# Kernel tuning notes

Measured on AMD Instinct MI355X. Metric: run time of the kernel, lower is better.

The kernel has to match this reference:

```python
import jax, jax.numpy as jnp
import numpy as np

D_MODEL = 1024
N_HEADS = 16
D_K = D_MODEL // N_HEADS
SCALE = float(np.sqrt(D_K))


def setup_inputs() -> dict:
    key = jax.random.key(0)
    ks = jax.random.split(key, 11)
    B, L, D = 2, 2048, D_MODEL
    s = 1.0 / np.sqrt(D)
    inp = {
        "q": jax.random.normal(ks[0], (B, L, D), dtype=jnp.float32),
        "k": jax.random.normal(ks[1], (B, L, D), dtype=jnp.float32),
        "v": jax.random.normal(ks[2], (B, L, D), dtype=jnp.float32),
        "Wq": jax.random.normal(ks[3], (D, D), dtype=jnp.float32) * s,
        "bq": jnp.zeros((D,), dtype=jnp.float32),
        "Wk": jax.random.normal(ks[4], (D, D), dtype=jnp.float32) * s,
        "bk": jnp.zeros((D,), dtype=jnp.float32),
        "Wv": jax.random.normal(ks[5], (D, D), dtype=jnp.float32) * s,
        "bv": jnp.zeros((D,), dtype=jnp.float32),
        "Wo": jax.random.normal(ks[6], (D, D), dtype=jnp.float32) * s,
        "bo": jnp.zeros((D,), dtype=jnp.float32),
    }
    return inp


def reference(q, k, v, Wq, bq, Wk, bk, Wv, bv, Wo, bo):
    B, L, D = q.shape
    H, Dk = N_HEADS, D_K
    # projections: [B,L,D] -> [B,H,L,Dk]
    def proj(x, W, b):
        y = x @ W + b
        return y.reshape(B, -1, H, Dk).transpose(0, 2, 1, 3)
    qh = proj(q, Wq, bq)
    kh = proj(k, Wk, bk)
    vh = proj(v, Wv, bv)
    # scores [B,H,Lq,Lk]
    scores = jnp.einsum("bhqd,bhkd->bhqk", qh, kh) / SCALE
    attn = jax.nn.softmax(scores, axis=-1)  # dropout=0.0 -> identity
    out = jnp.einsum("bhqk,bhkd->bhqd", attn, vh)
    out = out.transpose(0, 2, 1, 3).reshape(B, -1, D)
    return out @ Wo + bo
```

## Files before the change

### kernel.cpp

```cpp
#include <hip/hip_runtime.h>
#include <hip/hip_bf16.h>
#include <stdint.h>
#include <stddef.h>

typedef unsigned short ushortT;
typedef __attribute__((ext_vector_type(8))) short bf16x8s;
typedef __attribute__((ext_vector_type(4))) float f32x4;


__device__ __forceinline__ short f2bf(float f) {
  unsigned u = __float_as_uint(f);
  u += 0x7FFFu + ((u >> 16) & 1u);
  return (short)(u >> 16);
}
__device__ __forceinline__ float bf2f(ushortT s) {
  return __uint_as_float(((unsigned)s) << 16);
}

__device__ __forceinline__ bf16x8s load_a8(const void* A, int isf32, size_t off) {
  if (isf32) {
    const float4* p = (const float4*)((const float*)A + off);
    float4 x = p[0], y = p[1];
    bf16x8s r;
    r[0] = f2bf(x.x); r[1] = f2bf(x.y); r[2] = f2bf(x.z); r[3] = f2bf(x.w);
    r[4] = f2bf(y.x); r[5] = f2bf(y.y); r[6] = f2bf(y.z); r[7] = f2bf(y.w);
    return r;
  }
  return *(const bf16x8s*)((const ushortT*)A + off);
}

__device__ __forceinline__ void load_lds16(const ushortT* g, ushortT* l) {
  __builtin_amdgcn_global_load_lds(
      (const __attribute__((address_space(1))) void*)(g),
      (__attribute__((address_space(3))) void*)(l), 16, 0, 0);
}

__global__ void detect_dtype(const unsigned* __restrict__ q, int* __restrict__ flag) {
  __shared__ int cnt;
  if (threadIdx.x == 0) cnt = 0;
  __syncthreads();
  int c = 0;
  for (int i = threadIdx.x; i < 4096; i += 256) {
    float a = fabsf(__uint_as_float(q[i]));
    if (a > 1e-8f && a < 1e8f) c++;
  }
  atomicAdd(&cnt, c);
  __syncthreads();
  if (threadIdx.x == 0) *flag = (cnt > 2048) ? 1 : 0;
}

__global__ __launch_bounds__(256)
void convert3(const void* __restrict__ q, const void* __restrict__ k,
              const void* __restrict__ v, const int* __restrict__ flag,
              ushortT* __restrict__ Qc, ushortT* __restrict__ Kc,
              ushortT* __restrict__ Vc)
{
  const int isf32 = *flag;
  const int z = blockIdx.z;
  const void* src = (z == 0) ? q : (z == 1) ? k : v;
  ushortT* dst = (z == 0) ? Qc : (z == 1) ? Kc : Vc;
  const size_t i8 = ((size_t)blockIdx.x * 256 + threadIdx.x) * 8;
  *(bf16x8s*)(dst + i8) = load_a8(src, isf32, i8);
}

__global__ void transpose_w(const void* __restrict__ Wq, const void* __restrict__ Wk,
                            const void* __restrict__ Wv, const void* __restrict__ Wo,
                            const int* __restrict__ flag, ushortT* __restrict__ Wt)
{
  __shared__ __align__(16) ushortT t[32][33];
  const int isf32 = *flag;
  const int z = blockIdx.z;
  const void* W = (z == 0) ? Wq : (z == 1) ? Wk : (z == 2) ? Wv : Wo;
  ushortT* dst = Wt + (size_t)z * 1024 * 1024;
  const int x = blockIdx.x * 32, y = blockIdx.y * 32;
  const int tx = threadIdx.x, ty = threadIdx.y;
#pragma unroll
  for (int i = ty; i < 32; i += 8) {
    const size_t idx = (size_t)(y + i) * 1024 + x + tx;
    t[i][tx] = isf32 ? (ushortT)f2bf(((const float*)W)[idx])
                     : ((const ushortT*)W)[idx];
  }
  __syncthreads();
#pragma unroll
  for (int i = ty; i < 32; i += 8)
    dst[(size_t)(x + i) * 1024 + y + tx] = t[tx][i];
}

__device__ __forceinline__ void gemm_core_128(
    const ushortT* __restrict__ A, const ushortT* __restrict__ Bt,
    int K, ushortT* As, ushortT* Bs, f32x4 (&acc)[4][4], int m0, int n0)
{
  const int tid  = threadIdx.x;
  const int wave = tid >> 6, lane = tid & 63;
  const int wm = (wave & 1) << 6;
  const int wn = (wave >> 1) << 6;
  const int lr = lane & 15;
  const int lk = (lane >> 4) << 3;

#pragma unroll
  for (int mi = 0; mi < 4; ++mi)
#pragma unroll
    for (int ni = 0; ni < 4; ++ni)
      acc[mi][ni] = (f32x4){0.f, 0.f, 0.f, 0.f};

  for (int k0 = 0; k0 < K; k0 += 32) {
    __syncthreads();
#pragma unroll
    for (int i = 0; i < 2; ++i) {
      const int cc  = tid + (i << 8);
      const int row = cc >> 2;
      const int ko  = (cc & 3) << 3;
      load_lds16(A  + (size_t)(m0 + row) * K + k0 + ko, As + cc * 8);
      load_lds16(Bt + (size_t)(n0 + row) * K + k0 + ko, Bs + cc * 8);
    }
    __syncthreads();

    bf16x8s af[4], bfr[4];
#pragma unroll
    for (int i = 0; i < 4; ++i)
      af[i] = *(const bf16x8s*)(As + (wm + i * 16 + lr) * 32 + lk);
#pragma unroll
    for (int i = 0; i < 4; ++i)
      bfr[i] = *(const bf16x8s*)(Bs + (wn + i * 16 + lr) * 32 + lk);

#pragma unroll
    for (int mi = 0; mi < 4; ++mi)
#pragma unroll
      for (int ni = 0; ni < 4; ++ni)
        acc[mi][ni] = __builtin_amdgcn_mfma_f32_16x16x32_bf16(
            af[mi], bfr[ni], acc[mi][ni], 0, 0, 0);
  }
}

__global__ __launch_bounds__(256)
void proj_gemm(const ushortT* __restrict__ Qc, const ushortT* __restrict__ Kc,
               const ushortT* __restrict__ Vc, const ushortT* __restrict__ WtAll,
               const void* __restrict__ bq, const void* __restrict__ bk,
               const void* __restrict__ bv, const int* __restrict__ flag,
               ushortT* __restrict__ Qh, ushortT* __restrict__ Kh,
               ushortT* __restrict__ Vt)
{
  __shared__ __align__(16) ushortT As[128 * 32];
  __shared__ __align__(16) ushortT Bs[128 * 32];
  const int isf32 = *flag;
  const int which = blockIdx.z;
  const ushortT* A  = (which == 0) ? Qc : (which == 1) ? Kc : Vc;
  const ushortT* Bt = WtAll + (size_t)which * 1024 * 1024;
  const void* bias  = (which == 0) ? bq : (which == 1) ? bk : bv;
  const int m0 = blockIdx.x * 128, n0 = blockIdx.y * 128;

  f32x4 acc[4][4];
  gemm_core_128(A, Bt, 1024, As, Bs, acc, m0, n0);

  const int lane = threadIdx.x & 63, wave = threadIdx.x >> 6;
  const int wm = (wave & 1) << 6, wn = (wave >> 1) << 6;
  const int lr = lane & 15, quad = lane >> 4;
  const float QSCALE = 0.18033688011112042f;

#pragma unroll
  for (int ni = 0; ni < 4; ++ni) {
    const int n = n0 + wn + ni * 16 + lr;
    const float bias_v = isf32 ? ((const float*)bias)[n]
                               : bf2f(((const ushortT*)bias)[n]);
    const int h = n >> 6, d = n & 63;
#pragma unroll
    for (int mi = 0; mi < 4; ++mi) {
#pragma unroll
      for (int r = 0; r < 4; ++r) {
        const int m = m0 + wm + mi * 16 + quad * 4 + r;
        const int b = m >> 11, l = m & 2047;
        float val = acc[mi][ni][r] + bias_v;
        if (which == 0) val *= QSCALE;
        const ushortT o = (ushortT)f2bf(val);
        const size_t bh = (size_t)(b * 16 + h);
        if (which == 0)      Qh[(bh * 2048 + l) * 64 + d] = o;
        else if (which == 1) Kh[(bh * 2048 + l) * 64 + d] = o;
        else                 Vt[(bh * 64 + d) * 2048 + l] = o;
      }
    }
  }
}

__global__ __launch_bounds__(256)
void attn_kernel(const ushortT* __restrict__ Qh, const ushortT* __restrict__ Kh,
                 const ushortT* __restrict__ Vt, ushortT* __restrict__ Ob)
{
  const int b = blockIdx.z, h = blockIdx.y, qt = blockIdx.x;
  const int bh = b * 16 + h;
  const int wave = threadIdx.x >> 6, lane = threadIdx.x & 63;
  const int lr = lane & 15, quad = lane >> 4, lk = quad * 8;
  const int q0 = qt * 128 + wave * 32;

  const ushortT* Q = Qh + ((size_t)bh * 2048 + q0) * 64;
  const ushortT* K = Kh + (size_t)bh * 2048 * 64;
  const ushortT* V = Vt + (size_t)bh * 64 * 2048;

  __shared__ __align__(16) ushortT Ks[64 * 76];
  __shared__ __align__(16) ushortT Vs[64 * 76];
  __shared__ __align__(16) ushortT P4[4][32 * 76];
  ushortT* Pw = P4[wave];

  bf16x8s qf[2][2];
#pragma unroll
  for (int mt = 0; mt < 2; ++mt) {
    qf[mt][0] = *(const bf16x8s*)(Q + (mt * 16 + lr) * 64 + lk);
    qf[mt][1] = *(const bf16x8s*)(Q + (mt * 16 + lr) * 64 + 32 + lk);
  }

  f32x4 o[2][4];
#pragma unroll
  for (int mt = 0; mt < 2; ++mt)
#pragma unroll
    for (int nt = 0; nt < 4; ++nt) o[mt][nt] = (f32x4){0.f, 0.f, 0.f, 0.f};
  float lsum[2][4] = {{0.f, 0.f, 0.f, 0.f}, {0.f, 0.f, 0.f, 0.f}};

  const int tid = threadIdx.x;
  for (int kt = 0; kt < 2048; kt += 64) {
    bf16x8s kch[2], vch[2];
#pragma unroll
    for (int i = 0; i < 2; ++i) {
      const int cc  = tid + (i << 8);
      const int row = cc >> 3;
      const int c8  = (cc & 7) << 3;
      kch[i] = *(const bf16x8s*)(K + (size_t)(kt + row) * 64 + c8);
      vch[i] = *(const bf16x8s*)(V + (size_t)row * 2048 + kt + c8);
    }
    __syncthreads();
#pragma unroll
    for (int i = 0; i < 2; ++i) {
      const int cc  = tid + (i << 8);
      const int row = cc >> 3;
      const int c8  = (cc & 7) << 3;
      *(bf16x8s*)(Ks + row * 76 + c8) = kch[i];
      *(bf16x8s*)(Vs + row * 76 + c8) = vch[i];
    }
    __syncthreads();

    f32x4 s[2][4];
#pragma unroll
    for (int mt = 0; mt < 2; ++mt)
#pragma unroll
      for (int t = 0; t < 4; ++t) s[mt][t] = (f32x4){0.f, 0.f, 0.f, 0.f};
#pragma unroll
    for (int t = 0; t < 4; ++t) {
      const bf16x8s kf0 = *(const bf16x8s*)(Ks + (t * 16 + lr) * 76 + lk);
      const bf16x8s kf1 = *(const bf16x8s*)(Ks + (t * 16 + lr) * 76 + 32 + lk);
#pragma unroll
      for (int mt = 0; mt < 2; ++mt) {
        s[mt][t] = __builtin_amdgcn_mfma_f32_16x16x32_bf16(qf[mt][0], kf0, s[mt][t], 0, 0, 0);
        s[mt][t] = __builtin_amdgcn_mfma_f32_16x16x32_bf16(qf[mt][1], kf1, s[mt][t], 0, 0, 0);
      }
    }

#pragma unroll
    for (int mt = 0; mt < 2; ++mt)
#pragma unroll
      for (int t = 0; t < 4; ++t)
#pragma unroll
        for (int r = 0; r < 4; ++r) {
          const float p = __builtin_amdgcn_exp2f(s[mt][t][r]);
          lsum[mt][r] += p;
          Pw[(mt * 16 + quad * 4 + r) * 76 + t * 16 + lr] = (ushortT)f2bf(p);
        }
    asm volatile("s_waitcnt lgkmcnt(0)" ::: "memory");

    bf16x8s pf[2][2];
#pragma unroll
    for (int mt = 0; mt < 2; ++mt) {
      pf[mt][0] = *(const bf16x8s*)(Pw + (mt * 16 + lr) * 76 + lk);
      pf[mt][1] = *(const bf16x8s*)(Pw + (mt * 16 + lr) * 76 + 32 + lk);
    }
#pragma unroll
    for (int nt = 0; nt < 4; ++nt) {
      const bf16x8s vf0 = *(const bf16x8s*)(Vs + (nt * 16 + lr) * 76 + lk);
      const bf16x8s vf1 = *(const bf16x8s*)(Vs + (nt * 16 + lr) * 76 + 32 + lk);
#pragma unroll
      for (int mt = 0; mt < 2; ++mt) {
        o[mt][nt] = __builtin_amdgcn_mfma_f32_16x16x32_bf16(pf[mt][0], vf0, o[mt][nt], 0, 0, 0);
        o[mt][nt] = __builtin_amdgcn_mfma_f32_16x16x32_bf16(pf[mt][1], vf1, o[mt][nt], 0, 0, 0);
      }
    }
  }

  float inv[2][4];
#pragma unroll
  for (int mt = 0; mt < 2; ++mt)
#pragma unroll
    for (int r = 0; r < 4; ++r) {
      float s = lsum[mt][r];
      s += __shfl_xor(s, 1);
      s += __shfl_xor(s, 2);
      s += __shfl_xor(s, 4);
      s += __shfl_xor(s, 8);
      inv[mt][r] = 1.0f / s;
    }
#pragma unroll
  for (int mt = 0; mt < 2; ++mt)
#pragma unroll
    for (int nt = 0; nt < 4; ++nt) {
      const int dcol = h * 64 + nt * 16 + lr;
#pragma unroll
      for (int r = 0; r < 4; ++r) {
        const int l = q0 + mt * 16 + quad * 4 + r;
        Ob[((size_t)b * 2048 + l) * 1024 + dcol] =
            (ushortT)f2bf(o[mt][nt][r] * inv[mt][r]);
      }
    }
}

__global__ __launch_bounds__(256)
void out_gemm(const ushortT* __restrict__ Ob, const ushortT* __restrict__ Wto,
              const void* __restrict__ bo, const int* __restrict__ flag,
              void* __restrict__ C)
{
  __shared__ __align__(16) ushortT As[128 * 32];
  __shared__ __align__(16) ushortT Bs[128 * 32];
  const int isf32 = *flag;
  const int m0 = blockIdx.x * 128, n0 = blockIdx.y * 128;

  f32x4 acc[4][4];
  gemm_core_128(Ob, Wto, 1024, As, Bs, acc, m0, n0);

  const int lane = threadIdx.x & 63, wave = threadIdx.x >> 6;
  const int wm = (wave & 1) << 6, wn = (wave >> 1) << 6;
  const int lr = lane & 15, quad = lane >> 4;

#pragma unroll
  for (int ni = 0; ni < 4; ++ni) {
    const int n = n0 + wn + ni * 16 + lr;
    const float bias_v = isf32 ? ((const float*)bo)[n]
                               : bf2f(((const ushortT*)bo)[n]);
#pragma unroll
    for (int mi = 0; mi < 4; ++mi) {
#pragma unroll
      for (int r = 0; r < 4; ++r) {
        const int m = m0 + wm + mi * 16 + quad * 4 + r;
        const float val = acc[mi][ni][r] + bias_v;
        const size_t idx = (size_t)m * 1024 + n;
        if (isf32) ((float*)C)[idx] = val;
        else       ((ushortT*)C)[idx] = (ushortT)f2bf(val);
      }
    }
  }
}

extern "C" void kernel_launch(void* const* d_in, const int* in_sizes, int n_in,
                              void* d_out, int out_size, void* d_ws, size_t ws_size,
                              hipStream_t stream) {
  const void* q  = d_in[0];
  const void* k  = d_in[1];
  const void* v  = d_in[2];
  const void* Wq = d_in[3];
  const void* bq = d_in[4];
  const void* Wk = d_in[5];
  const void* bk = d_in[6];
  const void* Wv = d_in[7];
  const void* bv = d_in[8];
  const void* Wo = d_in[9];
  const void* bo = d_in[10];

  char* ws = (char*)d_ws;
  int*     flag = (int*)ws;
  ushortT* Wt = (ushortT*)(ws + (size_t)(1  << 20));
  ushortT* Qh = (ushortT*)(ws + (size_t)(9  << 20));
  ushortT* Kh = (ushortT*)(ws + (size_t)(17 << 20));
  ushortT* Vt = (ushortT*)(ws + (size_t)(25 << 20));
  ushortT* Qc = (ushortT*)(ws + (size_t)(33 << 20));
  ushortT* Kc = (ushortT*)(ws + (size_t)(41 << 20));
  ushortT* Vc = (ushortT*)(ws + (size_t)(49 << 20));
  ushortT* Ob = Qc;

  detect_dtype<<<1, 256, 0, stream>>>((const unsigned*)q, flag);
  convert3<<<dim3(2048, 1, 3), 256, 0, stream>>>(q, k, v, flag, Qc, Kc, Vc);
  transpose_w<<<dim3(32, 32, 4), dim3(32, 8), 0, stream>>>(Wq, Wk, Wv, Wo, flag, Wt);
  proj_gemm<<<dim3(32, 8, 3), 256, 0, stream>>>(Qc, Kc, Vc, Wt, bq, bk, bv,
                                                flag, Qh, Kh, Vt);
  attn_kernel<<<dim3(16, 16, 2), 256, 0, stream>>>(Qh, Kh, Vt, Ob);
  out_gemm<<<dim3(32, 8), 256, 0, stream>>>(Ob, Wt + (size_t)3 * 1024 * 1024,
                                            bo, flag, d_out);
}
```

Measured before the change: 271.9 us.

## Drop dtype detection, merge prep kernels, prefetch next K/V tile in attention

Removes the dtype-detection kernel and the runtime flag branches by hardcoding fp32 inputs and output. Merges the activation conversion and weight transpose into one prep launch, cutting two launches. In attention, the next K/V tile is loaded into registers while the current tile is computed, so global load latency overlaps with MFMA work. This costs extra registers, and the prep grid launches idle blocks for the weight slices.

```diff
diff --git a/kernel.cpp b/kernel.cpp
--- a/kernel.cpp
+++ b/kernel.cpp
@@ -13,20 +13,14 @@
   u += 0x7FFFu + ((u >> 16) & 1u);
   return (short)(u >> 16);
 }
-__device__ __forceinline__ float bf2f(ushortT s) {
-  return __uint_as_float(((unsigned)s) << 16);
-}
-
-__device__ __forceinline__ bf16x8s load_a8(const void* A, int isf32, size_t off) {
-  if (isf32) {
-    const float4* p = (const float4*)((const float*)A + off);
-    float4 x = p[0], y = p[1];
-    bf16x8s r;
-    r[0] = f2bf(x.x); r[1] = f2bf(x.y); r[2] = f2bf(x.z); r[3] = f2bf(x.w);
-    r[4] = f2bf(y.x); r[5] = f2bf(y.y); r[6] = f2bf(y.z); r[7] = f2bf(y.w);
-    return r;
-  }
-  return *(const bf16x8s*)((const ushortT*)A + off);
+
+__device__ __forceinline__ bf16x8s cvt8(const float* src) {
+  const float4* p = (const float4*)src;
+  float4 a = p[0], b = p[1];
+  bf16x8s r;
+  r[0] = f2bf(a.x); r[1] = f2bf(a.y); r[2] = f2bf(a.z); r[3] = f2bf(a.w);
+  r[4] = f2bf(b.x); r[5] = f2bf(b.y); r[6] = f2bf(b.z); r[7] = f2bf(b.w);
+  return r;
 }
 
 __device__ __forceinline__ void load_lds16(const ushortT* g, ushortT* l) {
@@ -35,55 +29,35 @@
       (__attribute__((address_space(3))) void*)(l), 16, 0, 0);
 }
 
-__global__ void detect_dtype(const unsigned* __restrict__ q, int* __restrict__ flag) {
-  __shared__ int cnt;
-  if (threadIdx.x == 0) cnt = 0;
-  __syncthreads();
-  int c = 0;
-  for (int i = threadIdx.x; i < 4096; i += 256) {
-    float a = fabsf(__uint_as_float(q[i]));
-    if (a > 1e-8f && a < 1e8f) c++;
-  }
-  atomicAdd(&cnt, c);
-  __syncthreads();
-  if (threadIdx.x == 0) *flag = (cnt > 2048) ? 1 : 0;
-}
-
 __global__ __launch_bounds__(256)
-void convert3(const void* __restrict__ q, const void* __restrict__ k,
-              const void* __restrict__ v, const int* __restrict__ flag,
-              ushortT* __restrict__ Qc, ushortT* __restrict__ Kc,
-              ushortT* __restrict__ Vc)
-{
-  const int isf32 = *flag;
+void prep(const float* __restrict__ q, const float* __restrict__ k,
+          const float* __restrict__ v,
+          const float* __restrict__ Wq, const float* __restrict__ Wk,
+          const float* __restrict__ Wv, const float* __restrict__ Wo,
+          ushortT* __restrict__ Qc, ushortT* __restrict__ Kc,
+          ushortT* __restrict__ Vc, ushortT* __restrict__ Wt)
+{
   const int z = blockIdx.z;
-  const void* src = (z == 0) ? q : (z == 1) ? k : v;
-  ushortT* dst = (z == 0) ? Qc : (z == 1) ? Kc : Vc;
-  const size_t i8 = ((size_t)blockIdx.x * 256 + threadIdx.x) * 8;
-  *(bf16x8s*)(dst + i8) = load_a8(src, isf32, i8);
-}
-
-__global__ void transpose_w(const void* __restrict__ Wq, const void* __restrict__ Wk,
-                            const void* __restrict__ Wv, const void* __restrict__ Wo,
-                            const int* __restrict__ flag, ushortT* __restrict__ Wt)
-{
-  __shared__ __align__(16) ushortT t[32][33];
-  const int isf32 = *flag;
-  const int z = blockIdx.z;
-  const void* W = (z == 0) ? Wq : (z == 1) ? Wk : (z == 2) ? Wv : Wo;
-  ushortT* dst = Wt + (size_t)z * 1024 * 1024;
-  const int x = blockIdx.x * 32, y = blockIdx.y * 32;
-  const int tx = threadIdx.x, ty = threadIdx.y;
-#pragma unroll
-  for (int i = ty; i < 32; i += 8) {
-    const size_t idx = (size_t)(y + i) * 1024 + x + tx;
-    t[i][tx] = isf32 ? (ushortT)f2bf(((const float*)W)[idx])
-                     : ((const ushortT*)W)[idx];
-  }
-  __syncthreads();
-#pragma unroll
-  for (int i = ty; i < 32; i += 8)
-    dst[(size_t)(x + i) * 1024 + y + tx] = t[tx][i];
+  if (z < 4) {
+    if (blockIdx.x >= 1024) return;
+    __shared__ __align__(16) ushortT t[32][33];
+    const float* W = (z == 0) ? Wq : (z == 1) ? Wk : (z == 2) ? Wv : Wo;
+    ushortT* dst = Wt + (size_t)z * 1024 * 1024;
+    const int x = (blockIdx.x & 31) * 32, y = (blockIdx.x >> 5) * 32;
+    const int tx = threadIdx.x & 31, ty = threadIdx.x >> 5;
+#pragma unroll
+    for (int i = ty; i < 32; i += 8)
+      t[i][tx] = (ushortT)f2bf(W[(size_t)(y + i) * 1024 + x + tx]);
+    __syncthreads();
+#pragma unroll
+    for (int i = ty; i < 32; i += 8)
+      dst[(size_t)(x + i) * 1024 + y + tx] = t[tx][i];
+  } else {
+    const float* src = (z == 4) ? q : (z == 5) ? k : v;
+    ushortT* dst = (z == 4) ? Qc : (z == 5) ? Kc : Vc;
+    const size_t i8 = ((size_t)blockIdx.x * 256 + threadIdx.x) * 8;
+    *(bf16x8s*)(dst + i8) = cvt8(src + i8);
+  }
 }
 
 __device__ __forceinline__ void gemm_core_128(
@@ -135,18 +109,17 @@
 __global__ __launch_bounds__(256)
 void proj_gemm(const ushortT* __restrict__ Qc, const ushortT* __restrict__ Kc,
                const ushortT* __restrict__ Vc, const ushortT* __restrict__ WtAll,
-               const void* __restrict__ bq, const void* __restrict__ bk,
-               const void* __restrict__ bv, const int* __restrict__ flag,
+               const float* __restrict__ bq, const float* __restrict__ bk,
+               const float* __restrict__ bv,
                ushortT* __restrict__ Qh, ushortT* __restrict__ Kh,
                ushortT* __restrict__ Vt)
 {
   __shared__ __align__(16) ushortT As[128 * 32];
   __shared__ __align__(16) ushortT Bs[128 * 32];
-  const int isf32 = *flag;
   const int which = blockIdx.z;
   const ushortT* A  = (which == 0) ? Qc : (which == 1) ? Kc : Vc;
   const ushortT* Bt = WtAll + (size_t)which * 1024 * 1024;
-  const void* bias  = (which == 0) ? bq : (which == 1) ? bk : bv;
+  const float* bias = (which == 0) ? bq : (which == 1) ? bk : bv;
   const int m0 = blockIdx.x * 128, n0 = blockIdx.y * 128;
 
   f32x4 acc[4][4];
@@ -160,8 +133,7 @@
 #pragma unroll
   for (int ni = 0; ni < 4; ++ni) {
     const int n = n0 + wn + ni * 16 + lr;
-    const float bias_v = isf32 ? ((const float*)bias)[n]
-                               : bf2f(((const ushortT*)bias)[n]);
+    const float bias_v = bias[n];
     const int h = n >> 6, d = n & 63;
 #pragma unroll
     for (int mi = 0; mi < 4; ++mi) {
@@ -215,26 +187,34 @@
   float lsum[2][4] = {{0.f, 0.f, 0.f, 0.f}, {0.f, 0.f, 0.f, 0.f}};
 
   const int tid = threadIdx.x;
+  const int srow = tid >> 3;
+  const int sc8  = (tid & 7) << 3;
+
+  bf16x8s kch[2], vch[2];
+#pragma unroll
+  for (int i = 0; i < 2; ++i) {
+    const int row = srow + i * 32;
+    kch[i] = *(const bf16x8s*)(K + (size_t)row * 64 + sc8);
+    vch[i] = *(const bf16x8s*)(V + (size_t)row * 2048 + sc8);
+  }
+
   for (int kt = 0; kt < 2048; kt += 64) {
-    bf16x8s kch[2], vch[2];
+    __syncthreads();
 #pragma unroll
     for (int i = 0; i < 2; ++i) {
-      const int cc  = tid + (i << 8);
-      const int row = cc >> 3;
-      const int c8  = (cc & 7) << 3;
-      kch[i] = *(const bf16x8s*)(K + (size_t)(kt + row) * 64 + c8);
-      vch[i] = *(const bf16x8s*)(V + (size_t)row * 2048 + kt + c8);
-    }
-    __syncthreads();
+      const int row = srow + i * 32;
+      *(bf16x8s*)(Ks + row * 76 + sc8) = kch[i];
+      *(bf16x8s*)(Vs + row * 76 + sc8) = vch[i];
+    }
+    __syncthreads();
+
+    const int kn = (kt + 64) & 2047;
 #pragma unroll
     for (int i = 0; i < 2; ++i) {
-      const int cc  = tid + (i << 8);
-      const int row = cc >> 3;
-      const int c8  = (cc & 7) << 3;
-      *(bf16x8s*)(Ks + row * 76 + c8) = kch[i];
-      *(bf16x8s*)(Vs + row * 76 + c8) = vch[i];
-    }
-    __syncthreads();
+      const int row = srow + i * 32;
+      kch[i] = *(const bf16x8s*)(K + (size_t)(kn + row) * 64 + sc8);
+      vch[i] = *(const bf16x8s*)(V + (size_t)row * 2048 + kn + sc8);
+    }
 
     f32x4 s[2][4];
 #pragma unroll
@@ -310,12 +290,10 @@
 
 __global__ __launch_bounds__(256)
 void out_gemm(const ushortT* __restrict__ Ob, const ushortT* __restrict__ Wto,
-              const void* __restrict__ bo, const int* __restrict__ flag,
-              void* __restrict__ C)
+              const float* __restrict__ bo, float* __restrict__ C)
 {
   __shared__ __align__(16) ushortT As[128 * 32];
   __shared__ __align__(16) ushortT Bs[128 * 32];
-  const int isf32 = *flag;
   const int m0 = blockIdx.x * 128, n0 = blockIdx.y * 128;
 
   f32x4 acc[4][4];
@@ -328,17 +306,13 @@
 #pragma unroll
   for (int ni = 0; ni < 4; ++ni) {
     const int n = n0 + wn + ni * 16 + lr;
-    const float bias_v = isf32 ? ((const float*)bo)[n]
-                               : bf2f(((const ushortT*)bo)[n]);
+    const float bias_v = bo[n];
 #pragma unroll
     for (int mi = 0; mi < 4; ++mi) {
 #pragma unroll
       for (int r = 0; r < 4; ++r) {
         const int m = m0 + wm + mi * 16 + quad * 4 + r;
-        const float val = acc[mi][ni][r] + bias_v;
-        const size_t idx = (size_t)m * 1024 + n;
-        if (isf32) ((float*)C)[idx] = val;
-        else       ((ushortT*)C)[idx] = (ushortT)f2bf(val);
+        C[(size_t)m * 1024 + n] = acc[mi][ni][r] + bias_v;
       }
     }
   }
@@ -347,35 +321,33 @@
 extern "C" void kernel_launch(void* const* d_in, const int* in_sizes, int n_in,
                               void* d_out, int out_size, void* d_ws, size_t ws_size,
                               hipStream_t stream) {
-  const void* q  = d_in[0];
-  const void* k  = d_in[1];
-  const void* v  = d_in[2];
-  const void* Wq = d_in[3];
-  const void* bq = d_in[4];
-  const void* Wk = d_in[5];
-  const void* bk = d_in[6];
-  const void* Wv = d_in[7];
-  const void* bv = d_in[8];
-  const void* Wo = d_in[9];
-  const void* bo = d_in[10];
+  const float* q  = (const float*)d_in[0];
+  const float* k  = (const float*)d_in[1];
+  const float* v  = (const float*)d_in[2];
+  const float* Wq = (const float*)d_in[3];
+  const float* bq = (const float*)d_in[4];
+  const float* Wk = (const float*)d_in[5];
+  const float* bk = (const float*)d_in[6];
+  const float* Wv = (const float*)d_in[7];
+  const float* bv = (const float*)d_in[8];
+  const float* Wo = (const float*)d_in[9];
+  const float* bo = (const float*)d_in[10];
 
   char* ws = (char*)d_ws;
-  int*     flag = (int*)ws;
-  ushortT* Wt = (ushortT*)(ws + (size_t)(1  << 20));
-  ushortT* Qh = (ushortT*)(ws + (size_t)(9  << 20));
-  ushortT* Kh = (ushortT*)(ws + (size_t)(17 << 20));
-  ushortT* Vt = (ushortT*)(ws + (size_t)(25 << 20));
-  ushortT* Qc = (ushortT*)(ws + (size_t)(33 << 20));
-  ushortT* Kc = (ushortT*)(ws + (size_t)(41 << 20));
-  ushortT* Vc = (ushortT*)(ws + (size_t)(49 << 20));
+  ushortT* Wt = (ushortT*)(ws);
+  ushortT* Qh = (ushortT*)(ws + (size_t)(8  << 20));
+  ushortT* Kh = (ushortT*)(ws + (size_t)(16 << 20));
+  ushortT* Vt = (ushortT*)(ws + (size_t)(24 << 20));
+  ushortT* Qc = (ushortT*)(ws + (size_t)(32 << 20));
+  ushortT* Kc = (ushortT*)(ws + (size_t)(40 << 20));
+  ushortT* Vc = (ushortT*)(ws + (size_t)(48 << 20));
   ushortT* Ob = Qc;
 
-  detect_dtype<<<1, 256, 0, stream>>>((const unsigned*)q, flag);
-  convert3<<<dim3(2048, 1, 3), 256, 0, stream>>>(q, k, v, flag, Qc, Kc, Vc);
-  transpose_w<<<dim3(32, 32, 4), dim3(32, 8), 0, stream>>>(Wq, Wk, Wv, Wo, flag, Wt);
+  prep<<<dim3(2048, 1, 7), 256, 0, stream>>>(q, k, v, Wq, Wk, Wv, Wo,
+                                             Qc, Kc, Vc, Wt);
   proj_gemm<<<dim3(32, 8, 3), 256, 0, stream>>>(Qc, Kc, Vc, Wt, bq, bk, bv,
-                                                flag, Qh, Kh, Vt);
+                                                Qh, Kh, Vt);
   attn_kernel<<<dim3(16, 16, 2), 256, 0, stream>>>(Qh, Kh, Vt, Ob);
   out_gemm<<<dim3(32, 8), 256, 0, stream>>>(Ob, Wt + (size_t)3 * 1024 * 1024,
-                                            bo, flag, d_out);
-}
+                                            bo, (float*)d_out);
+}
```

Result: faster. 265.6 us (-2.3%).
